# Performance work log

Hardware: AMD Instinct MI355X
Metric: run time of the kernel (lower is better)

## Reference

```python
import jax, jax.numpy as jnp
import numpy as np

B = 1048576
CARDS = np.array([2,2,2,2,2,3,3,4,4,4,4,4,4,5,5,5,5,5,5,5,2,2,2,2,2,2,2,2,2], dtype=np.int32)
NBR = 29  # number of categorical branches
EPS = 1e-5


def setup_inputs() -> dict:
    key = jax.random.key(0)
    ks = jax.random.split(key, 24)
    inp = {}
    inp['xcon'] = jax.random.normal(ks[0], (B, 7), dtype=jnp.float32)
    raw = jax.random.randint(ks[1], (B, NBR), 0, 5, dtype=jnp.int32)
    inp['xcat'] = raw % jnp.asarray(CARDS)[None, :]  # in-range per-branch indices
    s6 = 1.0 / np.sqrt(6.0)
    inp['emb_tables'] = jax.random.normal(ks[2], (NBR, 5, 6), dtype=jnp.float32)
    inp['w1'] = jax.random.normal(ks[3], (NBR, 6, 6), dtype=jnp.float32) * s6
    inp['b1'] = jax.random.normal(ks[4], (NBR, 6), dtype=jnp.float32) * s6
    inp['w2'] = jax.random.normal(ks[5], (NBR, 6), dtype=jnp.float32) * s6
    inp['b2'] = jax.random.normal(ks[6], (NBR,), dtype=jnp.float32) * s6
    inp['cbn_g'] = jnp.ones((7,), jnp.float32)
    inp['cbn_b'] = jnp.zeros((7,), jnp.float32)
    inp['cbn_m'] = jax.random.normal(ks[7], (7,), jnp.float32) * 0.1
    inp['cbn_v'] = jnp.ones((7,), jnp.float32) + 0.1 * jax.random.uniform(ks[8], (7,))
    dims = [(36, 36), (18, 36), (9, 18), (2, 9)]
    for i, (o, ic) in enumerate(dims, 1):
        s = 1.0 / np.sqrt(ic)
        inp[f'fc{i}_w'] = jax.random.normal(ks[8 + 2 * i], (o, ic), jnp.float32) * s
        inp[f'fc{i}_b'] = jax.random.normal(ks[9 + 2 * i], (o,), jnp.float32) * s
    for i, d in zip([1, 2, 3], [36, 18, 9]):
        inp[f'bn{i}_g'] = jnp.ones((d,), jnp.float32)
        inp[f'bn{i}_b'] = jnp.zeros((d,), jnp.float32)
        inp[f'bn{i}_m'] = jax.random.normal(jax.random.fold_in(key, 100 + i), (d,), jnp.float32) * 0.1
        inp[f'bn{i}_v'] = jnp.ones((d,), jnp.float32) + 0.1 * jax.random.uniform(jax.random.fold_in(key, 200 + i), (d,))
    return inp


def _bn(x, g, b, m, v):
    return (x - m) * jax.lax.rsqrt(v + EPS) * g + b


def reference(xcon, xcat, emb_tables, w1, b1, w2, b2,
              cbn_g, cbn_b, cbn_m, cbn_v,
              fc1_w, fc1_b, bn1_g, bn1_b, bn1_m, bn1_v,
              fc2_w, fc2_b, bn2_g, bn2_b, bn2_m, bn2_v,
              fc3_w, fc3_b, bn3_g, bn3_b, bn3_m, bn3_v,
              fc4_w, fc4_b):
    # Batched gather over all 29 branches: [B,29,6]
    emb = emb_tables[jnp.arange(NBR)[None, :], xcat]
    # Per-branch tiny MLP, fused as batched GEMMs
    h = jax.nn.relu(jnp.einsum('bjd,jde->bje', emb, w1) + b1)   # [B,29,6]
    xcatemb = jnp.einsum('bjd,jd->bj', h, w2) + b2              # [B,29]
    # (catdo_layer dropout is identity in eval mode)
    xcon_n = _bn(xcon, cbn_g, cbn_b, cbn_m, cbn_v)              # BatchNorm1d(7), eval
    xin = jnp.concatenate([xcon_n, xcatemb], axis=1)            # [B,36]
    h1 = jax.nn.relu(_bn(xin @ fc1_w.T + fc1_b, bn1_g, bn1_b, bn1_m, bn1_v))
    h2 = jax.nn.relu(_bn(h1 @ fc2_w.T + fc2_b, bn2_g, bn2_b, bn2_m, bn2_v))
    h3 = jax.nn.relu(_bn(h2 @ fc3_w.T + fc3_b, bn3_g, bn3_b, bn3_m, bn3_v))
    logits = h3 @ fc4_w.T + fc4_b                               # [B,2]
    return jax.nn.softmax(logits, axis=1)
```

## Files before the change

kernel.cpp:

```cpp
#include <hip/hip_runtime.h>

typedef _Float16 f16x8 __attribute__((ext_vector_type(8)));
typedef __fp16 fp16x2 __attribute__((ext_vector_type(2)));
typedef float f32x4 __attribute__((ext_vector_type(4)));

#define NTHR 256
constexpr float EPS = 1e-5f;
constexpr int NBLOCKS = 4096;

#define TAB_B   0
#define W1_B    1024
#define W2_B    7168
#define W3_B    11264
#define W4_B    12736

__device__ __forceinline__ ushort f16bits(float x) {
    union { _Float16 h; ushort u; } c; c.h = (_Float16)x; return c.u;
}
__device__ __forceinline__ uint pk2(float a, float b) {
    union { fp16x2 h; uint u; } c; c.h = __builtin_amdgcn_cvt_pkrtz(a, b); return c.u;
}
__device__ __forceinline__ uint pkrelu(float a, float b) {
    return pk2(fmaxf(a, 0.f), fmaxf(b, 0.f));
}
__device__ __forceinline__ f16x8 mk8(uint a, uint b, uint c, uint d) {
    union { uint u[4]; f16x8 v; } f;
    f.u[0] = a; f.u[1] = b; f.u[2] = c; f.u[3] = d;
    return f.v;
}
__device__ __forceinline__ f16x8 ldw_frag(const ushort* wp, int m, int stride, int kb, int g) {
    const ushort* p = wp + m * stride + kb + 4 * g;
    uint2 lo = *(const uint2*)p;
    uint2 hi = *(const uint2*)(p + 16);
    return mk8(lo.x, lo.y, hi.x, hi.y);
}

__global__ __launch_bounds__(NTHR) void prep_kernel(
    const float* __restrict__ embt, const float* __restrict__ w1,
    const float* __restrict__ b1,   const float* __restrict__ w2,
    const float* __restrict__ b2,
    const float* __restrict__ cbn_g, const float* __restrict__ cbn_b,
    const float* __restrict__ cbn_m, const float* __restrict__ cbn_v,
    const float* __restrict__ f1w, const float* __restrict__ f1b,
    const float* __restrict__ f2w, const float* __restrict__ f2b,
    const float* __restrict__ f3w, const float* __restrict__ f3b,
    const float* __restrict__ f4w, const float* __restrict__ f4b,
    const float* __restrict__ bn1g, const float* __restrict__ bn1b,
    const float* __restrict__ bn1m, const float* __restrict__ bn1v,
    const float* __restrict__ bn2g, const float* __restrict__ bn2b,
    const float* __restrict__ bn2m, const float* __restrict__ bn2v,
    const float* __restrict__ bn3g, const float* __restrict__ bn3b,
    const float* __restrict__ bn3m, const float* __restrict__ bn3v,
    char* __restrict__ ws)
{
    const int t = threadIdx.x;
    ushort* tab = (ushort*)(ws + TAB_B);
    ushort* w1o = (ushort*)(ws + W1_B);
    ushort* w2o = (ushort*)(ws + W2_B);
    ushort* w3o = (ushort*)(ws + W3_B);
    float* w4o = (float*)(ws + W4_B);

    for (int i = t; i < 232; i += NTHR) {
        int j = i / 8, c = i % 8;
        float xe = 0.f;
        if (c < 5) {
            xe = b2[j];
            for (int e = 0; e < 6; e++) {
                float a = b1[j * 6 + e];
                for (int d = 0; d < 6; d++)
                    a += embt[(j * 5 + c) * 6 + d] * w1[j * 36 + d * 6 + e];
                xe += fmaxf(a, 0.f) * w2[j * 6 + e];
            }
        }
        tab[i] = f16bits(xe);
    }
    for (int i = t; i < 3072; i += NTHR) {
        int n = i / 64, k = i % 64;
        float v = 0.f;
        if (n < 36) {
            float s1 = bn1g[n] * rsqrtf(bn1v[n] + EPS);
            if (k < 36) {
                v = f1w[n * 36 + k] * s1;
                if (k < 7) v *= cbn_g[k] * rsqrtf(cbn_v[k] + EPS);
            } else if (k == 36) {
                v = f1b[n] * s1 + bn1b[n] - bn1m[n] * s1;
                for (int kk = 0; kk < 7; kk++) {
                    float cs = cbn_g[kk] * rsqrtf(cbn_v[kk] + EPS);
                    float ct = cbn_b[kk] - cbn_m[kk] * cs;
                    v += f1w[n * 36 + kk] * s1 * ct;
                }
            }
        } else if (n == 36 && k == 36) {
            v = 1.f;
        }
        w1o[i] = f16bits(v);
    }
    for (int i = t; i < 2048; i += NTHR) {
        int n = i / 64, k = i % 64;
        float v = 0.f;
        if (n < 18) {
            float s = bn2g[n] * rsqrtf(bn2v[n] + EPS);
            if (k < 36) v = f2w[n * 36 + k] * s;
            else if (k == 36) v = f2b[n] * s + bn2b[n] - bn2m[n] * s;
        } else if (n == 18 && k == 36) {
            v = 1.f;
        }
        w2o[i] = f16bits(v);
    }
    for (int i = t; i < 512; i += NTHR) {
        int n = i / 32, k = i % 32;
        float v = 0.f;
        if (n < 9) {
            float s = bn3g[n] * rsqrtf(bn3v[n] + EPS);
            if (k < 18) v = f3w[n * 18 + k] * s;
            else if (k == 18) v = f3b[n] * s + bn3b[n] - bn3m[n] * s;
        } else if (n == 9 && k == 18) {
            v = 1.f;
        }
        w3o[i] = f16bits(v);
    }
    if (t < 16) w4o[t] = (t < 9) ? (f4w[9 + t] - f4w[t]) : (t == 9 ? (f4b[1] - f4b[0]) : 0.f);
}

#define XSTRIDE 72

__global__ __launch_bounds__(NTHR, 4) void recovery_net_kernel(
    const float* __restrict__ xcon, const int* __restrict__ xcat,
    const char* __restrict__ ws, float2* __restrict__ out)
{
    __shared__ __align__(16) char s_x[256 * XSTRIDE];
    __shared__ uint s_catp[1856];
    __shared__ ushort s_tab[4][232];

    const int t = threadIdx.x;
    const int lane = t & 63, w = t >> 6;
    const int l15 = lane & 15, gq = lane >> 4;
    const int rb = w * 64;

    const float* xrow = xcon + ((size_t)blockIdx.x * 256 + t) * 7;
    float v0 = xrow[0], v1 = xrow[1], v2 = xrow[2], v3 = xrow[3];
    float v4 = xrow[4], v5 = xrow[5], v6 = xrow[6];

    for (int idx = lane; idx < 116; idx += 64)
        ((uint*)s_tab[w])[idx] = ((const uint*)(ws + TAB_B))[idx];

    {
        const int4* src = (const int4*)(xcat + ((size_t)blockIdx.x * 256 + rb) * 29);
        for (int idx = lane; idx < 464; idx += 64) {
            int4 v = src[idx];
            s_catp[w * 464 + idx] =
                (uint)(v.x & 0xff) | ((uint)(v.y & 0xff) << 8) |
                ((uint)(v.z & 0xff) << 16) | ((uint)(v.w & 0xff) << 24);
        }
    }
    asm volatile("s_waitcnt lgkmcnt(0)" ::: "memory");

    {
        const unsigned char* myc = (const unsigned char*)s_catp + w * 1856 + lane * 29;
        const ushort* tb = s_tab[w];
        ushort th[29];
#pragma unroll
        for (int j = 0; j < 29; j++) th[j] = tb[j * 8 + (int)myc[j]];
        uint wd[18];
        wd[0] = pk2(v0, v1);
        wd[1] = pk2(v2, v3);
        wd[2] = pk2(v4, v5);
        wd[3] = (uint)f16bits(v6) | ((uint)th[0] << 16);
#pragma unroll
        for (int k = 0; k < 14; k++)
            wd[4 + k] = (uint)th[1 + 2 * k] | ((uint)th[2 + 2 * k] << 16);
        char* xb = s_x + t * XSTRIDE;
#pragma unroll
        for (int j = 0; j < 9; j++)
            *(uint2*)(xb + 8 * j) = make_uint2(wd[2 * j], wd[2 * j + 1]);
    }
    asm volatile("s_waitcnt lgkmcnt(0)" ::: "memory");

    const ushort* w1p = (const ushort*)(ws + W1_B);
    const ushort* w2p = (const ushort*)(ws + W2_B);
    const ushort* w3p = (const ushort*)(ws + W3_B);
    f16x8 a1[3][2], a2[2][2], a3;
#pragma unroll
    for (int mt = 0; mt < 3; mt++) {
        a1[mt][0] = ldw_frag(w1p, mt * 16 + l15, 64, 0, gq);
        a1[mt][1] = ldw_frag(w1p, mt * 16 + l15, 64, 32, gq);
    }
#pragma unroll
    for (int mt = 0; mt < 2; mt++) {
        a2[mt][0] = ldw_frag(w2p, mt * 16 + l15, 64, 0, gq);
        a2[mt][1] = ldw_frag(w2p, mt * 16 + l15, 64, 32, gq);
    }
    a3 = ldw_frag(w3p, l15, 32, 0, gq);
    const float4 w4v = *(const float4*)((const float*)(ws + W4_B) + 4 * gq);

#pragma unroll
    for (int bt = 0; bt < 4; bt++) {
        const char* xr = s_x + (rb + 16 * bt + l15) * XSTRIDE;
        uint2 q0 = *(const uint2*)(xr + 8 * gq);
        uint2 q1 = *(const uint2*)(xr + 32 + 8 * gq);
        uint2 q2 = *(const uint2*)(xr + 64);
        f16x8 xb0 = mk8(q0.x, q0.y, q1.x, q1.y);
        uint cw0 = (gq == 0) ? q2.x : (gq == 1 ? 0x00003C00u : 0u);
        uint cw1 = (gq == 0) ? q2.y : 0u;
        f16x8 xb1 = mk8(cw0, cw1, 0u, 0u);

        f32x4 c10 = {0.f, 0.f, 0.f, 0.f};
        f32x4 c11 = {0.f, 0.f, 0.f, 0.f};
        f32x4 c12 = {0.f, 0.f, 0.f, 0.f};
        c10 = __builtin_amdgcn_mfma_f32_16x16x32_f16(a1[0][0], xb0, c10, 0, 0, 0);
        c11 = __builtin_amdgcn_mfma_f32_16x16x32_f16(a1[1][0], xb0, c11, 0, 0, 0);
        c12 = __builtin_amdgcn_mfma_f32_16x16x32_f16(a1[2][0], xb0, c12, 0, 0, 0);
        c10 = __builtin_amdgcn_mfma_f32_16x16x32_f16(a1[0][1], xb1, c10, 0, 0, 0);
        c11 = __builtin_amdgcn_mfma_f32_16x16x32_f16(a1[1][1], xb1, c11, 0, 0, 0);
        c12 = __builtin_amdgcn_mfma_f32_16x16x32_f16(a1[2][1], xb1, c12, 0, 0, 0);

        f16x8 h0 = mk8(pkrelu(c10.x, c10.y), pkrelu(c10.z, c10.w),
                       pkrelu(c11.x, c11.y), pkrelu(c11.z, c11.w));
        f16x8 h1 = mk8(pkrelu(c12.x, c12.y), pkrelu(c12.z, c12.w), 0u, 0u);

        f32x4 c20 = {0.f, 0.f, 0.f, 0.f};
        f32x4 c21 = {0.f, 0.f, 0.f, 0.f};
        c20 = __builtin_amdgcn_mfma_f32_16x16x32_f16(a2[0][0], h0, c20, 0, 0, 0);
        c21 = __builtin_amdgcn_mfma_f32_16x16x32_f16(a2[1][0], h0, c21, 0, 0, 0);
        c20 = __builtin_amdgcn_mfma_f32_16x16x32_f16(a2[0][1], h1, c20, 0, 0, 0);
        c21 = __builtin_amdgcn_mfma_f32_16x16x32_f16(a2[1][1], h1, c21, 0, 0, 0);

        f16x8 h2 = mk8(pkrelu(c20.x, c20.y), pkrelu(c20.z, c20.w),
                       pkrelu(c21.x, c21.y), pkrelu(c21.z, c21.w));
        f32x4 c3 = {0.f, 0.f, 0.f, 0.f};
        c3 = __builtin_amdgcn_mfma_f32_16x16x32_f16(a3, h2, c3, 0, 0, 0);

        float part = fmaxf(c3.x, 0.f) * w4v.x + fmaxf(c3.y, 0.f) * w4v.y +
                     fmaxf(c3.z, 0.f) * w4v.z + fmaxf(c3.w, 0.f) * w4v.w;
        part += __shfl_xor(part, 16);
        part += __shfl_xor(part, 32);
        float p1v = 1.f / (1.f + __expf(-part));
        if (gq == 0)
            out[(size_t)blockIdx.x * 256 + rb + 16 * bt + l15] = make_float2(1.f - p1v, p1v);
    }
}

extern "C" void kernel_launch(void* const* d_in, const int* in_sizes, int n_in,
                              void* d_out, int out_size, void* d_ws, size_t ws_size,
                              hipStream_t stream) {
    (void)in_sizes; (void)n_in; (void)ws_size; (void)out_size;
    char* ws = (char*)d_ws;
    prep_kernel<<<1, NTHR, 0, stream>>>(
        (const float*)d_in[2],  (const float*)d_in[3],
        (const float*)d_in[4],  (const float*)d_in[5],
        (const float*)d_in[6],
        (const float*)d_in[7],  (const float*)d_in[8],
        (const float*)d_in[9],  (const float*)d_in[10],
        (const float*)d_in[11], (const float*)d_in[12],
        (const float*)d_in[13], (const float*)d_in[14],
        (const float*)d_in[15], (const float*)d_in[16],
        (const float*)d_in[17], (const float*)d_in[18],
        (const float*)d_in[19], (const float*)d_in[20],
        (const float*)d_in[21], (const float*)d_in[22],
        (const float*)d_in[23], (const float*)d_in[24],
        (const float*)d_in[25], (const float*)d_in[26],
        (const float*)d_in[27], (const float*)d_in[28],
        (const float*)d_in[29], (const float*)d_in[30],
        ws);
    recovery_net_kernel<<<NBLOCKS, NTHR, 0, stream>>>(
        (const float*)d_in[0], (const int*)d_in[1], ws, (float2*)d_out);
}
```

Measured before the change: 81.64 us.

## Gather MFMA operands directly from global, dropping LDS staging of inputs

Removes the shared-memory staging of xcon and packed xcat. Each lane now loads its own feature indices from global and looks up the embedding table to build the MFMA B operand directly, and the fc1 weight columns are permuted to match the new lane-to-feature mapping. The table stride becomes 10 per branch. Layer 2 and 3 weight fragments are reloaded inside the loop to cut register pressure, and launch bounds go from 4 to 5 waves' worth of blocks for higher occupancy. The trade-off is uncoalesced strided global loads of xcat and xcon per lane, plus repeated weight loads.

```diff
diff --git a/kernel.cpp b/kernel.cpp
--- a/kernel.cpp
+++ b/kernel.cpp
@@ -60,8 +60,8 @@
     ushort* w3o = (ushort*)(ws + W3_B);
     float* w4o = (float*)(ws + W4_B);
 
-    for (int i = t; i < 232; i += NTHR) {
-        int j = i / 8, c = i % 8;
+    for (int i = t; i < 290; i += NTHR) {
+        int j = i / 10, c = i % 10;
         float xe = 0.f;
         if (c < 5) {
             xe = b2[j];
@@ -76,13 +76,14 @@
     }
     for (int i = t; i < 3072; i += NTHR) {
         int n = i / 64, k = i % 64;
+        int feat = (k < 32) ? (8 * ((k >> 2) & 3) + 4 * (k >> 4) + (k & 3)) : k;
         float v = 0.f;
         if (n < 36) {
             float s1 = bn1g[n] * rsqrtf(bn1v[n] + EPS);
-            if (k < 36) {
-                v = f1w[n * 36 + k] * s1;
-                if (k < 7) v *= cbn_g[k] * rsqrtf(cbn_v[k] + EPS);
-            } else if (k == 36) {
+            if (feat < 36) {
+                v = f1w[n * 36 + feat] * s1;
+                if (feat < 7) v *= cbn_g[feat] * rsqrtf(cbn_v[feat] + EPS);
+            } else if (feat == 36) {
                 v = f1b[n] * s1 + bn1b[n] - bn1m[n] * s1;
                 for (int kk = 0; kk < 7; kk++) {
                     float cs = cbn_g[kk] * rsqrtf(cbn_v[kk] + EPS);
@@ -122,86 +123,64 @@
     if (t < 16) w4o[t] = (t < 9) ? (f4w[9 + t] - f4w[t]) : (t == 9 ? (f4b[1] - f4b[0]) : 0.f);
 }
 
-#define XSTRIDE 72
-
-__global__ __launch_bounds__(NTHR, 4) void recovery_net_kernel(
+__global__ __launch_bounds__(NTHR, 5) void recovery_net_kernel(
     const float* __restrict__ xcon, const int* __restrict__ xcat,
     const char* __restrict__ ws, float2* __restrict__ out)
 {
-    __shared__ __align__(16) char s_x[256 * XSTRIDE];
-    __shared__ uint s_catp[1856];
-    __shared__ ushort s_tab[4][232];
+    __shared__ ushort s_tab[4][292];
 
     const int t = threadIdx.x;
     const int lane = t & 63, w = t >> 6;
     const int l15 = lane & 15, gq = lane >> 4;
-    const int rb = w * 64;
-
-    const float* xrow = xcon + ((size_t)blockIdx.x * 256 + t) * 7;
-    float v0 = xrow[0], v1 = xrow[1], v2 = xrow[2], v3 = xrow[3];
-    float v4 = xrow[4], v5 = xrow[5], v6 = xrow[6];
-
-    for (int idx = lane; idx < 116; idx += 64)
+    const int bRow = blockIdx.x * 256 + w * 64;
+
+    for (int idx = lane; idx < 145; idx += 64)
         ((uint*)s_tab[w])[idx] = ((const uint*)(ws + TAB_B))[idx];
-
-    {
-        const int4* src = (const int4*)(xcat + ((size_t)blockIdx.x * 256 + rb) * 29);
-        for (int idx = lane; idx < 464; idx += 64) {
-            int4 v = src[idx];
-            s_catp[w * 464 + idx] =
-                (uint)(v.x & 0xff) | ((uint)(v.y & 0xff) << 8) |
-                ((uint)(v.z & 0xff) << 16) | ((uint)(v.w & 0xff) << 24);
-        }
-    }
-    asm volatile("s_waitcnt lgkmcnt(0)" ::: "memory");
-
-    {
-        const unsigned char* myc = (const unsigned char*)s_catp + w * 1856 + lane * 29;
-        const ushort* tb = s_tab[w];
-        ushort th[29];
-#pragma unroll
-        for (int j = 0; j < 29; j++) th[j] = tb[j * 8 + (int)myc[j]];
-        uint wd[18];
-        wd[0] = pk2(v0, v1);
-        wd[1] = pk2(v2, v3);
-        wd[2] = pk2(v4, v5);
-        wd[3] = (uint)f16bits(v6) | ((uint)th[0] << 16);
-#pragma unroll
-        for (int k = 0; k < 14; k++)
-            wd[4 + k] = (uint)th[1 + 2 * k] | ((uint)th[2 + 2 * k] << 16);
-        char* xb = s_x + t * XSTRIDE;
-#pragma unroll
-        for (int j = 0; j < 9; j++)
-            *(uint2*)(xb + 8 * j) = make_uint2(wd[2 * j], wd[2 * j + 1]);
-    }
-    asm volatile("s_waitcnt lgkmcnt(0)" ::: "memory");
 
     const ushort* w1p = (const ushort*)(ws + W1_B);
     const ushort* w2p = (const ushort*)(ws + W2_B);
     const ushort* w3p = (const ushort*)(ws + W3_B);
-    f16x8 a1[3][2], a2[2][2], a3;
+    f16x8 a1[3][2];
 #pragma unroll
     for (int mt = 0; mt < 3; mt++) {
         a1[mt][0] = ldw_frag(w1p, mt * 16 + l15, 64, 0, gq);
         a1[mt][1] = ldw_frag(w1p, mt * 16 + l15, 64, 32, gq);
     }
-#pragma unroll
-    for (int mt = 0; mt < 2; mt++) {
-        a2[mt][0] = ldw_frag(w2p, mt * 16 + l15, 64, 0, gq);
-        a2[mt][1] = ldw_frag(w2p, mt * 16 + l15, 64, 32, gq);
-    }
-    a3 = ldw_frag(w3p, l15, 32, 0, gq);
     const float4 w4v = *(const float4*)((const float*)(ws + W4_B) + 4 * gq);
+
+    asm volatile("s_waitcnt lgkmcnt(0)" ::: "memory");
+    __builtin_amdgcn_wave_barrier();
+    const ushort* tb = s_tab[w];
 
 #pragma unroll
     for (int bt = 0; bt < 4; bt++) {
-        const char* xr = s_x + (rb + 16 * bt + l15) * XSTRIDE;
-        uint2 q0 = *(const uint2*)(xr + 8 * gq);
-        uint2 q1 = *(const uint2*)(xr + 32 + 8 * gq);
-        uint2 q2 = *(const uint2*)(xr + 64);
-        f16x8 xb0 = mk8(q0.x, q0.y, q1.x, q1.y);
-        uint cw0 = (gq == 0) ? q2.x : (gq == 1 ? 0x00003C00u : 0u);
-        uint cw1 = (gq == 0) ? q2.y : 0u;
+        const int r = bRow + 16 * bt + l15;
+        const int* kp = xcat + (size_t)r * 29;
+        uint u0, u1, u2, u3, cw0 = 0, cw1 = 0;
+        if (gq == 0) {
+            const float* cp = xcon + (size_t)r * 7;
+            float f0 = cp[0], f1 = cp[1], f2 = cp[2], f3 = cp[3];
+            float f4 = cp[4], f5 = cp[5], f6 = cp[6];
+            int m7 = kp[0], e0 = kp[25], e1 = kp[26], e2 = kp[27], e3 = kp[28];
+            u0 = pk2(f0, f1);
+            u1 = pk2(f2, f3);
+            u2 = pk2(f4, f5);
+            u3 = (uint)f16bits(f6) | ((uint)tb[m7] << 16);
+            cw0 = (uint)tb[250 + e0] | ((uint)tb[260 + e1] << 16);
+            cw1 = (uint)tb[270 + e2] | ((uint)tb[280 + e3] << 16);
+        } else {
+            const int jb = 8 * gq - 7;
+            const int* bp = kp + jb;
+            int m0 = bp[0], m1 = bp[1], m2 = bp[2], m3 = bp[3];
+            int m4 = bp[4], m5 = bp[5], m6 = bp[6], m7 = bp[7];
+            const ushort* tj = tb + jb * 10;
+            u0 = (uint)tj[m0] | ((uint)tj[10 + m1] << 16);
+            u1 = (uint)tj[20 + m2] | ((uint)tj[30 + m3] << 16);
+            u2 = (uint)tj[40 + m4] | ((uint)tj[50 + m5] << 16);
+            u3 = (uint)tj[60 + m6] | ((uint)tj[70 + m7] << 16);
+            cw0 = (gq == 1) ? 0x00003C00u : 0u;
+        }
+        f16x8 xb0 = mk8(u0, u1, u2, u3);
         f16x8 xb1 = mk8(cw0, cw1, 0u, 0u);
 
         f32x4 c10 = {0.f, 0.f, 0.f, 0.f};
@@ -220,15 +199,24 @@
 
         f32x4 c20 = {0.f, 0.f, 0.f, 0.f};
         f32x4 c21 = {0.f, 0.f, 0.f, 0.f};
-        c20 = __builtin_amdgcn_mfma_f32_16x16x32_f16(a2[0][0], h0, c20, 0, 0, 0);
-        c21 = __builtin_amdgcn_mfma_f32_16x16x32_f16(a2[1][0], h0, c21, 0, 0, 0);
-        c20 = __builtin_amdgcn_mfma_f32_16x16x32_f16(a2[0][1], h1, c20, 0, 0, 0);
-        c21 = __builtin_amdgcn_mfma_f32_16x16x32_f16(a2[1][1], h1, c21, 0, 0, 0);
+        {
+            f16x8 b0 = ldw_frag(w2p, l15,      64, 0, gq);
+            f16x8 b1 = ldw_frag(w2p, 16 + l15, 64, 0, gq);
+            c20 = __builtin_amdgcn_mfma_f32_16x16x32_f16(b0, h0, c20, 0, 0, 0);
+            c21 = __builtin_amdgcn_mfma_f32_16x16x32_f16(b1, h0, c21, 0, 0, 0);
+            b0 = ldw_frag(w2p, l15,      64, 32, gq);
+            b1 = ldw_frag(w2p, 16 + l15, 64, 32, gq);
+            c20 = __builtin_amdgcn_mfma_f32_16x16x32_f16(b0, h1, c20, 0, 0, 0);
+            c21 = __builtin_amdgcn_mfma_f32_16x16x32_f16(b1, h1, c21, 0, 0, 0);
+        }
 
         f16x8 h2 = mk8(pkrelu(c20.x, c20.y), pkrelu(c20.z, c20.w),
                        pkrelu(c21.x, c21.y), pkrelu(c21.z, c21.w));
         f32x4 c3 = {0.f, 0.f, 0.f, 0.f};
-        c3 = __builtin_amdgcn_mfma_f32_16x16x32_f16(a3, h2, c3, 0, 0, 0);
+        {
+            f16x8 a3 = ldw_frag(w3p, l15, 32, 0, gq);
+            c3 = __builtin_amdgcn_mfma_f32_16x16x32_f16(a3, h2, c3, 0, 0, 0);
+        }
 
         float part = fmaxf(c3.x, 0.f) * w4v.x + fmaxf(c3.y, 0.f) * w4v.y +
                      fmaxf(c3.z, 0.f) * w4v.z + fmaxf(c3.w, 0.f) * w4v.w;
@@ -236,7 +224,7 @@
         part += __shfl_xor(part, 32);
         float p1v = 1.f / (1.f + __expf(-part));
         if (gq == 0)
-            out[(size_t)blockIdx.x * 256 + rb + 16 * bt + l15] = make_float2(1.f - p1v, p1v);
+            out[r] = make_float2(1.f - p1v, p1v);
     }
 }
 
```

Result: no change. 82.38 us (+0.9%).
